# Performance work log

Measured on AMD Instinct MI355X. Metric: run time of the kernel, lower is better.

Reference implementation:

```python
import jax, jax.numpy as jnp
import numpy as np
from jax import lax

EMBED_DIM = 1024
NUM_HEADS = 8
KEY_DIM = EMBED_DIM // NUM_HEADS  # 128
B, H, W = 2, 48, 48
N = H * W


def _rope(t, sin, cos):
    # t: [..., d]; sin/cos broadcastable to t
    x1 = t[..., ::2]
    x2 = t[..., 1::2]
    rot = jnp.stack([-x2, x1], axis=-1).reshape(t.shape)  # interleave (-x2, x1)
    return t * cos - rot * sin


def setup_inputs() -> dict:
    key = jax.random.key(0)
    ks = jax.random.split(key, 16)
    C = EMBED_DIM
    w = 0.02
    return {
        "x": jax.random.normal(ks[0], (B, H, W, C), jnp.float32),
        "sin": jax.random.normal(ks[1], (H, W, KEY_DIM), jnp.float32),
        "cos": jax.random.normal(ks[2], (H, W, KEY_DIM), jnp.float32),
        "mask": jax.random.normal(ks[3], (NUM_HEADS, N, N), jnp.float32),
        "Wq": jax.random.normal(ks[4], (C, C), jnp.float32) * w,
        "bq": jax.random.normal(ks[5], (C,), jnp.float32) * w,
        "Wk": jax.random.normal(ks[6], (C, C), jnp.float32) * w,
        "bk": jax.random.normal(ks[7], (C,), jnp.float32) * w,
        "Wv": jax.random.normal(ks[8], (C, C), jnp.float32) * w,
        "bv": jax.random.normal(ks[9], (C,), jnp.float32) * w,
        "lepe_w": jax.random.normal(ks[10], (5, 5, 1, C), jnp.float32) * w,  # HWIO, groups=C
        "lepe_b": jax.random.normal(ks[11], (C,), jnp.float32) * w,
        "Wo": jax.random.normal(ks[12], (C, C), jnp.float32) * w,
        "bo": jnp.zeros((C,), jnp.float32),
    }


def reference(x, sin, cos, mask, Wq, bq, Wk, bk, Wv, bv, lepe_w, lepe_b, Wo, bo):
    Bb, Hh, Ww, C = x.shape
    nh, kd = NUM_HEADS, KEY_DIM
    scaling = kd ** -0.5

    q = x @ Wq.T + bq                     # [B,H,W,C]
    k = (x @ Wk.T + bk) * scaling         # [B,H,W,C]
    v = x @ Wv.T + bv                     # [B,H,W,C]

    # depthwise 5x5 lepe on NHWC
    lepe = lax.conv_general_dilated(
        v, lepe_w, window_strides=(1, 1), padding="SAME",
        dimension_numbers=("NHWC", "HWIO", "NHWC"),
        feature_group_count=C,
    ) + lepe_b

    # [B,H,W,C] -> [B,nh,H,W,kd]
    qh = q.reshape(Bb, Hh, Ww, nh, kd).transpose(0, 3, 1, 2, 4)
    kh = k.reshape(Bb, Hh, Ww, nh, kd).transpose(0, 3, 1, 2, 4)

    sin_ = sin[None, None]  # [1,1,H,W,kd]
    cos_ = cos[None, None]
    qh = _rope(qh, sin_, cos_)
    kh = _rope(kh, sin_, cos_)

    qf = qh.reshape(Bb, nh, Hh * Ww, kd)  # [B,nh,N,kd]
    kf = kh.reshape(Bb, nh, Hh * Ww, kd)
    vf = v.reshape(Bb, Hh, Ww, nh, kd).transpose(0, 3, 1, 2, 4).reshape(Bb, nh, Hh * Ww, kd)

    attn = jnp.einsum("bhnd,bhmd->bhnm", qf, kf) + mask  # [B,nh,N,N]
    attn = jax.nn.softmax(attn, axis=-1)
    out = jnp.einsum("bhnm,bhmd->bhnd", attn, vf)         # [B,nh,N,kd]

    out = out.transpose(0, 2, 1, 3).reshape(Bb, Hh, Ww, nh * kd)
    out = out + lepe
    return out @ Wo.T + bo
```

## Files before the change

kernel.cpp:

```cpp
#include <hip/hip_runtime.h>
#include <hip/hip_bf16.h>
#include <stdint.h>

typedef __bf16 bf16_t;
typedef __bf16 bf16x8 __attribute__((ext_vector_type(8)));
typedef __bf16 bf16x4 __attribute__((ext_vector_type(4)));
typedef float f32x4 __attribute__((ext_vector_type(4)));
typedef unsigned int u32x4 __attribute__((ext_vector_type(4)));

#define MFMA16(A, B, C) __builtin_amdgcn_mfma_f32_16x16x32_bf16(A, B, C, 0, 0, 0)

__device__ inline void dma16(const void* g, void* l) {
    __builtin_amdgcn_global_load_lds(
        (const __attribute__((address_space(1))) unsigned int*)g,
        (__attribute__((address_space(3))) unsigned int*)l, 16, 0, 0);
}

__device__ inline unsigned pack2(float a, float b) {
    unsigned short ua = __builtin_bit_cast(unsigned short, (bf16_t)a);
    unsigned short ub = __builtin_bit_cast(unsigned short, (bf16_t)b);
    return (unsigned)ua | ((unsigned)ub << 16);
}

__global__ __launch_bounds__(256)
void cvt_kernel(const float* __restrict__ in, bf16_t* __restrict__ outp, int n8)
{
    int i = blockIdx.x * 256 + threadIdx.x;
    if (i >= n8) return;
    const float* p = in + (size_t)i * 8;
    f32x4 a = *(const f32x4*)p;
    f32x4 b = *(const f32x4*)(p + 4);
    bf16x8 r;
    r[0] = (bf16_t)a[0]; r[1] = (bf16_t)a[1]; r[2] = (bf16_t)a[2]; r[3] = (bf16_t)a[3];
    r[4] = (bf16_t)b[0]; r[5] = (bf16_t)b[1]; r[6] = (bf16_t)b[2]; r[7] = (bf16_t)b[3];
    *(bf16x8*)(outp + (size_t)i * 8) = r;
}

__global__ __launch_bounds__(256)
void cvt4_kernel(const float* __restrict__ W0, const float* __restrict__ W1,
                 const float* __restrict__ W2, const float* __restrict__ W3,
                 bf16_t* __restrict__ outp)
{
    int i = blockIdx.x * 256 + threadIdx.x;
    int sel = i >> 17;
    int j = i & 131071;
    const float* src = sel == 0 ? W0 : sel == 1 ? W1 : sel == 2 ? W2 : W3;
    const float* p = src + (size_t)j * 8;
    f32x4 a = *(const f32x4*)p;
    f32x4 b = *(const f32x4*)(p + 4);
    bf16x8 r;
    r[0] = (bf16_t)a[0]; r[1] = (bf16_t)a[1]; r[2] = (bf16_t)a[2]; r[3] = (bf16_t)a[3];
    r[4] = (bf16_t)b[0]; r[5] = (bf16_t)b[1]; r[6] = (bf16_t)b[2]; r[7] = (bf16_t)b[3];
    *(bf16x8*)(outp + (size_t)i * 8) = r;
}

__device__ __forceinline__
void gemm_core(const bf16_t* __restrict__ A, const bf16_t* __restrict__ W,
               const float* __restrict__ bias, void* __restrict__ outp,
               int mode, float scale,
               const float* __restrict__ sinp, const float* __restrict__ cosp,
               int m0, int n0, char* lds)
{
    const int K = 1024;
    const int t = threadIdx.x;
    const int w = t >> 6, l = t & 63;
    const int wm = w >> 1, wn = w & 1;
    const int lr = l & 15;
    const int kch = (l >> 4) * 8;

    const f32x4 zz = {0.f, 0.f, 0.f, 0.f};
    f32x4 acc[4][4];
#pragma unroll
    for (int i = 0; i < 4; i++)
#pragma unroll
        for (int j = 0; j < 4; j++) acc[i][j] = zz;

#pragma unroll
    for (int i = 0; i < 2; i++) {
        int f = w * 2 + i;
        dma16(A + (size_t)(m0 + f * 16 + lr) * K + kch, lds + f * 1024);
        dma16(W + (size_t)(n0 + f * 16 + lr) * K + kch, lds + 8192 + f * 1024);
    }
    __syncthreads();

    int bo = 0;
    for (int k0 = 0; k0 < K; k0 += 32) {
        int kn = k0 + 32;
        if (kn < K) {
            int nb = bo ^ 16384;
#pragma unroll
            for (int i = 0; i < 2; i++) {
                int f = w * 2 + i;
                dma16(A + (size_t)(m0 + f * 16 + lr) * K + kn + kch, lds + nb + f * 1024);
                dma16(W + (size_t)(n0 + f * 16 + lr) * K + kn + kch, lds + nb + 8192 + f * 1024);
            }
        }
        bf16x8 af[4], bfg[4];
#pragma unroll
        for (int mt = 0; mt < 4; mt++)
            af[mt] = *(const bf16x8*)(lds + bo + ((wm * 4 + mt) * 64 + l) * 16);
#pragma unroll
        for (int nt = 0; nt < 4; nt++)
            bfg[nt] = *(const bf16x8*)(lds + bo + 8192 + ((wn * 4 + nt) * 64 + l) * 16);
#pragma unroll
        for (int mt = 0; mt < 4; mt++)
#pragma unroll
            for (int nt = 0; nt < 4; nt++)
                acc[mt][nt] = MFMA16(af[mt], bfg[nt], acc[mt][nt]);
        __syncthreads();
        bo ^= 16384;
    }

    const int quad = l >> 4, lc = l & 15;
#pragma unroll
    for (int mt = 0; mt < 4; mt++) {
#pragma unroll
        for (int nt = 0; nt < 4; nt++) {
            int gn = n0 + wn * 64 + nt * 16 + lc;
            float bv = bias[gn];
            int gm0 = m0 + wm * 64 + mt * 16 + quad * 4;
            if (mode == 0) {
                float* o32 = (float*)outp;
#pragma unroll
                for (int r = 0; r < 4; r++)
                    o32[(size_t)(gm0 + r) * 1024 + gn] = acc[mt][nt][r] + bv;
            } else if (mode == 1) {
                bf16_t* ob = (bf16_t*)outp;
                int h = gn >> 7, d = gn & 127;
#pragma unroll
                for (int r = 0; r < 4; r++) {
                    int gm = gm0 + r;
                    int b = gm / 2304;
                    int pos = gm - b * 2304;
                    float val = acc[mt][nt][r] + bv;
                    float pv = __shfl_xor(val, 1);
                    float sn = sinp[pos * 128 + d];
                    float cs = cosp[pos * 128 + d];
                    float res = (d & 1) ? (val * cs - pv * sn) : (val * cs + pv * sn);
                    ob[(((size_t)b * 8 + h) * 2304 + pos) * 128 + d] = (bf16_t)(res * scale);
                }
            } else {
                bf16_t* ob = (bf16_t*)outp;
                int h = gn >> 7, d = gn & 127;
                int b = gm0 / 2304;
                int pos0 = gm0 - b * 2304;
                bf16x4 s4;
#pragma unroll
                for (int r = 0; r < 4; r++)
                    s4[r] = (bf16_t)(acc[mt][nt][r] + bv);
                *(bf16x4*)(ob + (((size_t)b * 8 + h) * 128 + d) * 2304 + pos0) = s4;
            }
        }
    }
}

__global__ __launch_bounds__(256)
void gemm_bt_kernel(const bf16_t* __restrict__ A, const bf16_t* __restrict__ W,
                    const float* __restrict__ bias, void* __restrict__ outp,
                    int mode, float scale,
                    const float* __restrict__ sinp, const float* __restrict__ cosp)
{
    __shared__ __align__(16) char lds[32768];
    gemm_core(A, W, bias, outp, mode, scale, sinp, cosp,
              blockIdx.x * 128, blockIdx.y * 128, lds);
}

__global__ __launch_bounds__(256)
void gemm_qkv_kernel(const bf16_t* __restrict__ A, const bf16_t* __restrict__ Wall,
                     const float* __restrict__ bq, const float* __restrict__ bk,
                     const float* __restrict__ bv,
                     void* __restrict__ qb, void* __restrict__ kb, void* __restrict__ vtb,
                     const float* __restrict__ sinp, const float* __restrict__ cosp,
                     float kscale)
{
    __shared__ __align__(16) char lds[32768];
    int ny = blockIdx.y;
    int third = ny >> 3;
    int n0 = (ny & 7) * 128;
    const bf16_t* W = Wall + (size_t)third * 1048576;
    const float* bias = third == 0 ? bq : third == 1 ? bk : bv;
    void* outp = third == 0 ? qb : third == 1 ? kb : vtb;
    int mode = third == 2 ? 2 : 1;
    float scale = third == 1 ? kscale : 1.0f;
    gemm_core(A, W, bias, outp, mode, scale, sinp, cosp, blockIdx.x * 128, n0, lds);
}

__global__ __launch_bounds__(256)
void attn_kernel(const bf16_t* __restrict__ q, const bf16_t* __restrict__ k,
                 const bf16_t* __restrict__ vt, const float* __restrict__ mask,
                 bf16_t* __restrict__ o)
{
    const int N = 2304;
    __shared__ __align__(16) char lds[65536];

    const int t = threadIdx.x;
    const int w = t >> 6, l = t & 63;
    const int quad = l >> 4, lc = l & 15;

    const int bh = blockIdx.y;
    const int b = bh >> 3, h = bh & 7;
    const int q0 = blockIdx.x * 64;
    const int qrow = q0 + w * 16 + lc;

    const bf16_t* qb = q + (size_t)bh * N * 128;
    const bf16_t* kb = k + (size_t)bh * N * 128;
    const bf16_t* vtb = vt + (size_t)bh * 128 * N;
    const float* mq = mask + (size_t)h * N * N + (size_t)qrow * N + quad * 4;

    bf16x8 qf[4];
#pragma unroll
    for (int kc = 0; kc < 4; kc++)
        qf[kc] = *(const bf16x8*)(qb + (size_t)qrow * 128 + kc * 32 + quad * 8);

#pragma unroll
    for (int i = 0; i < 4; i++) {
        int f = w * 4 + i;
        dma16(kb + (size_t)((f >> 2) * 16 + lc) * 128 + (f & 3) * 32 + quad * 8,
              lds + f * 1024);
        dma16(vtb + (size_t)((f >> 1) * 16 + lc) * N + (f & 1) * 32 + quad * 8,
              lds + 16384 + f * 1024);
    }
    f32x4 mv[4];
#pragma unroll
    for (int nt = 0; nt < 4; nt++)
        mv[nt] = *(const f32x4*)(mq + nt * 16);
    __syncthreads();

    const f32x4 zz = {0.f, 0.f, 0.f, 0.f};
    float Mr = -1e30f, Lr = 0.f;
    f32x4 Oacc[8];
#pragma unroll
    for (int i = 0; i < 8; i++) Oacc[i] = zz;

    int bo = 0;
    for (int kv0 = 0; kv0 < N; kv0 += 64) {
        int nxt = kv0 + 64;
        f32x4 mvn[4];
        if (nxt < N) {
            int nb = bo ^ 32768;
#pragma unroll
            for (int i = 0; i < 4; i++) {
                int f = w * 4 + i;
                dma16(kb + (size_t)(nxt + (f >> 2) * 16 + lc) * 128 + (f & 3) * 32 + quad * 8,
                      lds + nb + f * 1024);
                dma16(vtb + (size_t)((f >> 1) * 16 + lc) * N + nxt + (f & 1) * 32 + quad * 8,
                      lds + nb + 16384 + f * 1024);
            }
#pragma unroll
            for (int nt = 0; nt < 4; nt++)
                mvn[nt] = *(const f32x4*)(mq + nxt + nt * 16);
        }

        const char* Ks = lds + bo;
        const char* Vts = lds + bo + 16384;

        f32x4 s[4];
#pragma unroll
        for (int nt = 0; nt < 4; nt++) {
            f32x4 a = zz;
#pragma unroll
            for (int kc = 0; kc < 4; kc++) {
                bf16x8 kf = *(const bf16x8*)(Ks + ((nt * 4 + kc) * 64 + l) * 16);
                a = MFMA16(kf, qf[kc], a);
            }
            s[nt] = a + mv[nt];
        }

        float mx = fmaxf(fmaxf(fmaxf(s[0][0], s[0][1]), fmaxf(s[0][2], s[0][3])),
                         fmaxf(fmaxf(s[1][0], s[1][1]), fmaxf(s[1][2], s[1][3])));
        mx = fmaxf(mx, fmaxf(fmaxf(fmaxf(s[2][0], s[2][1]), fmaxf(s[2][2], s[2][3])),
                             fmaxf(fmaxf(s[3][0], s[3][1]), fmaxf(s[3][2], s[3][3]))));
        mx = fmaxf(mx, __shfl_xor(mx, 16));
        mx = fmaxf(mx, __shfl_xor(mx, 32));
        float mnew = fmaxf(Mr, mx);
        float alpha = __expf(Mr - mnew);
        Mr = mnew;

        float rs = 0.f;
        unsigned pw[4][2];
#pragma unroll
        for (int nt = 0; nt < 4; nt++) {
            float p0 = __expf(s[nt][0] - mnew);
            float p1 = __expf(s[nt][1] - mnew);
            float p2 = __expf(s[nt][2] - mnew);
            float p3 = __expf(s[nt][3] - mnew);
            rs += (p0 + p1) + (p2 + p3);
            pw[nt][0] = pack2(p0, p1);
            pw[nt][1] = pack2(p2, p3);
        }
        rs += __shfl_xor(rs, 16);
        rs += __shfl_xor(rs, 32);
        Lr = Lr * alpha + rs;

#pragma unroll
        for (int dt = 0; dt < 8; dt++)
#pragma unroll
            for (int r = 0; r < 4; r++)
                Oacc[dt][r] *= alpha;

#pragma unroll
        for (int pc = 0; pc < 2; pc++) {
            u32x4 wv;
#pragma unroll
            for (int jp = 0; jp < 4; jp++) {
                int src = ((quad & 1) * 2 + (jp >> 1)) * 16 + lc;
                int t0 = __shfl((int)pw[pc * 2 + 0][jp & 1], src);
                int t1 = __shfl((int)pw[pc * 2 + 1][jp & 1], src);
                wv[jp] = (quad >> 1) ? (unsigned)t1 : (unsigned)t0;
            }
            bf16x8 pf = __builtin_bit_cast(bf16x8, wv);
#pragma unroll
            for (int dt = 0; dt < 8; dt++) {
                bf16x8 vf = *(const bf16x8*)(Vts + ((dt * 2 + pc) * 64 + l) * 16);
                Oacc[dt] = MFMA16(vf, pf, Oacc[dt]);
            }
        }

        __syncthreads();
        if (nxt < N) {
#pragma unroll
            for (int nt = 0; nt < 4; nt++) mv[nt] = mvn[nt];
            bo ^= 32768;
        }
    }

    float inv = 1.f / Lr;
#pragma unroll
    for (int dt = 0; dt < 8; dt++) {
        bf16x4 s4;
#pragma unroll
        for (int r = 0; r < 4; r++) s4[r] = (bf16_t)(Oacc[dt][r] * inv);
        *(bf16x4*)(o + ((size_t)b * N + qrow) * 1024 + h * 128 + dt * 16 + quad * 4) = s4;
    }
}

__global__ __launch_bounds__(256)
void lepe_kernel(const bf16_t* __restrict__ vt, const float* __restrict__ wgt,
                 const float* __restrict__ lb, const bf16_t* __restrict__ o,
                 bf16_t* __restrict__ ab)
{
    __shared__ __align__(16) bf16_t sv[5 * 48 * 128];
    const int bh = blockIdx.y;
    const int b = bh >> 3, h = bh & 7;
    const int y0 = blockIdx.x;
    const int t = threadIdx.x;

#pragma unroll
    for (int it = 0; it < 15; it++) {
        int idx = t + it * 256;
        int ck = idx % 6;
        int dy = idx / 6;
        int d = dy & 127, yloc = dy >> 7;
        int y = y0 - 2 + yloc;
        bf16x8 vvv;
#pragma unroll
        for (int j = 0; j < 8; j++) vvv[j] = (bf16_t)0.f;
        if (y >= 0 && y < 48)
            vvv = *(const bf16x8*)(vt + ((size_t)bh * 128 + d) * 2304 + y * 48 + ck * 8);
        int x0 = ck * 8;
#pragma unroll
        for (int j = 0; j < 8; j++)
            sv[(yloc * 48 + x0 + j) * 128 + d] = vvv[j];
    }
    __syncthreads();

    const int d0 = (t & 15) * 8;
    const int xb = t >> 4;
    float acc[3][8];
    f32x4 b0 = *(const f32x4*)(lb + h * 128 + d0);
    f32x4 b1 = *(const f32x4*)(lb + h * 128 + d0 + 4);
#pragma unroll
    for (int c = 0; c < 3; c++)
#pragma unroll
        for (int j = 0; j < 4; j++) { acc[c][j] = b0[j]; acc[c][4 + j] = b1[j]; }

#pragma unroll
    for (int ky = 0; ky < 5; ky++) {
#pragma unroll
        for (int kx = 0; kx < 5; kx++) {
            const float* wp = wgt + (size_t)(ky * 5 + kx) * 1024 + h * 128 + d0;
            f32x4 w0 = *(const f32x4*)wp;
            f32x4 w1 = *(const f32x4*)(wp + 4);
#pragma unroll
            for (int c = 0; c < 3; c++) {
                int xx = xb + c * 16 + kx - 2;
                if (xx < 0 || xx >= 48) continue;
                bf16x8 vv = *(const bf16x8*)(&sv[(ky * 48 + xx) * 128 + d0]);
#pragma unroll
                for (int j = 0; j < 4; j++) {
                    acc[c][j]     += (float)vv[j]     * w0[j];
                    acc[c][4 + j] += (float)vv[4 + j] * w1[j];
                }
            }
        }
    }
#pragma unroll
    for (int c = 0; c < 3; c++) {
        int x = xb + c * 16;
        size_t off = ((size_t)b * 2304 + y0 * 48 + x) * 1024 + h * 128 + d0;
        bf16x8 ov = *(const bf16x8*)(o + off);
        bf16x8 res;
#pragma unroll
        for (int j = 0; j < 8; j++) res[j] = (bf16_t)(acc[c][j] + (float)ov[j]);
        *(bf16x8*)(ab + off) = res;
    }
}

extern "C" void kernel_launch(void* const* d_in, const int* in_sizes, int n_in,
                              void* d_out, int out_size, void* d_ws, size_t ws_size,
                              hipStream_t stream)
{
    const float* x    = (const float*)d_in[0];
    const float* sin_ = (const float*)d_in[1];
    const float* cos_ = (const float*)d_in[2];
    const float* mask = (const float*)d_in[3];
    const float* Wq   = (const float*)d_in[4];
    const float* bq   = (const float*)d_in[5];
    const float* Wk   = (const float*)d_in[6];
    const float* bk   = (const float*)d_in[7];
    const float* Wv   = (const float*)d_in[8];
    const float* bv   = (const float*)d_in[9];
    const float* lw   = (const float*)d_in[10];
    const float* lb   = (const float*)d_in[11];
    const float* Wo   = (const float*)d_in[12];
    const float* bo   = (const float*)d_in[13];

    const size_t NB = (size_t)2 * 2304 * 1024;

    bf16_t* dout_b = (bf16_t*)d_out;
    bf16_t* x16 = dout_b;
    bf16_t* vtb = dout_b + NB;
    bf16_t* ob  = dout_b;

    bf16_t* qb   = (bf16_t*)d_ws;
    bf16_t* kb   = qb + NB;
    bf16_t* wbuf = kb + NB;
    bf16_t* ab   = qb;

    dim3 blk(256);
    const float kscale = 0.08838834764831845f;

    cvt_kernel<<<2304, blk, 0, stream>>>(x, x16, 589824);
    cvt4_kernel<<<2048, blk, 0, stream>>>(Wq, Wk, Wv, Wo, wbuf);
    gemm_qkv_kernel<<<dim3(36, 24), blk, 0, stream>>>(x16, wbuf, bq, bk, bv,
                                                      qb, kb, vtb, sin_, cos_, kscale);
    attn_kernel<<<dim3(36, 16), blk, 0, stream>>>(qb, kb, vtb, mask, ob);
    lepe_kernel<<<dim3(48, 16), blk, 0, stream>>>(vtb, lw, lb, ob, ab);
    gemm_bt_kernel<<<dim3(36, 8), blk, 0, stream>>>(ab, wbuf + 3 * 1048576, bo,
                                                    d_out, 0, 1.0f, nullptr, nullptr);
}
```

Measured before the change: 565.9 us.

## Split attention KV range across two wave groups and shrink GEMM M-tiles to 64

The attention kernel now runs 512 threads per block. Two groups of four waves each process half of the key/value sequence, and their partial softmax states (max, sum, output) are merged through LDS at the end. Blocks are also remapped so batch pairs sharing the same mask rows are adjacent, which aims to improve mask reuse in cache. The K/V double-buffer prefetch is replaced by a synchronous load for each tile, so the kernel now relies on more resident waves to hide latency. The GEMMs switch from 128-row to 64-row tiles, doubling the grid to improve CU occupancy, at the cost of less operand reuse per block.

```diff
diff --git a/kernel.cpp b/kernel.cpp
--- a/kernel.cpp
+++ b/kernel.cpp
@@ -55,13 +55,14 @@
 }
 
 __device__ __forceinline__
-void gemm_core(const bf16_t* __restrict__ A, const bf16_t* __restrict__ W,
-               const float* __restrict__ bias, void* __restrict__ outp,
-               int mode, float scale,
-               const float* __restrict__ sinp, const float* __restrict__ cosp,
-               int m0, int n0, char* lds)
+void gemm_core64(const bf16_t* __restrict__ A, const bf16_t* __restrict__ W,
+                 const float* __restrict__ bias, void* __restrict__ outp,
+                 int mode, float scale,
+                 const float* __restrict__ sinp, const float* __restrict__ cosp,
+                 int m0, int n0, char* lds)
 {
     const int K = 1024;
+    const int ASZ = 4096, BUF = 12288;
     const int t = threadIdx.x;
     const int w = t >> 6, l = t & 63;
     const int wm = w >> 1, wn = w & 1;
@@ -69,17 +70,17 @@
     const int kch = (l >> 4) * 8;
 
     const f32x4 zz = {0.f, 0.f, 0.f, 0.f};
-    f32x4 acc[4][4];
-#pragma unroll
-    for (int i = 0; i < 4; i++)
+    f32x4 acc[2][4];
+#pragma unroll
+    for (int i = 0; i < 2; i++)
 #pragma unroll
         for (int j = 0; j < 4; j++) acc[i][j] = zz;
 
+    dma16(A + (size_t)(m0 + w * 16 + lr) * K + kch, lds + w * 1024);
 #pragma unroll
     for (int i = 0; i < 2; i++) {
         int f = w * 2 + i;
-        dma16(A + (size_t)(m0 + f * 16 + lr) * K + kch, lds + f * 1024);
-        dma16(W + (size_t)(n0 + f * 16 + lr) * K + kch, lds + 8192 + f * 1024);
+        dma16(W + (size_t)(n0 + f * 16 + lr) * K + kch, lds + ASZ + f * 1024);
     }
     __syncthreads();
 
@@ -87,38 +88,38 @@
     for (int k0 = 0; k0 < K; k0 += 32) {
         int kn = k0 + 32;
         if (kn < K) {
-            int nb = bo ^ 16384;
+            int nb = bo ^ BUF;
+            dma16(A + (size_t)(m0 + w * 16 + lr) * K + kn + kch, lds + nb + w * 1024);
 #pragma unroll
             for (int i = 0; i < 2; i++) {
                 int f = w * 2 + i;
-                dma16(A + (size_t)(m0 + f * 16 + lr) * K + kn + kch, lds + nb + f * 1024);
-                dma16(W + (size_t)(n0 + f * 16 + lr) * K + kn + kch, lds + nb + 8192 + f * 1024);
-            }
-        }
-        bf16x8 af[4], bfg[4];
-#pragma unroll
-        for (int mt = 0; mt < 4; mt++)
-            af[mt] = *(const bf16x8*)(lds + bo + ((wm * 4 + mt) * 64 + l) * 16);
+                dma16(W + (size_t)(n0 + f * 16 + lr) * K + kn + kch, lds + nb + ASZ + f * 1024);
+            }
+        }
+        bf16x8 af[2], bfg[4];
+#pragma unroll
+        for (int mt = 0; mt < 2; mt++)
+            af[mt] = *(const bf16x8*)(lds + bo + ((wm * 2 + mt) * 64 + l) * 16);
 #pragma unroll
         for (int nt = 0; nt < 4; nt++)
-            bfg[nt] = *(const bf16x8*)(lds + bo + 8192 + ((wn * 4 + nt) * 64 + l) * 16);
-#pragma unroll
-        for (int mt = 0; mt < 4; mt++)
+            bfg[nt] = *(const bf16x8*)(lds + bo + ASZ + ((wn * 4 + nt) * 64 + l) * 16);
+#pragma unroll
+        for (int mt = 0; mt < 2; mt++)
 #pragma unroll
             for (int nt = 0; nt < 4; nt++)
                 acc[mt][nt] = MFMA16(af[mt], bfg[nt], acc[mt][nt]);
         __syncthreads();
-        bo ^= 16384;
+        bo ^= BUF;
     }
 
     const int quad = l >> 4, lc = l & 15;
 #pragma unroll
-    for (int mt = 0; mt < 4; mt++) {
+    for (int mt = 0; mt < 2; mt++) {
 #pragma unroll
         for (int nt = 0; nt < 4; nt++) {
             int gn = n0 + wn * 64 + nt * 16 + lc;
             float bv = bias[gn];
-            int gm0 = m0 + wm * 64 + mt * 16 + quad * 4;
+            int gm0 = m0 + wm * 32 + mt * 16 + quad * 4;
             if (mode == 0) {
                 float* o32 = (float*)outp;
 #pragma unroll
@@ -160,9 +161,9 @@
                     int mode, float scale,
                     const float* __restrict__ sinp, const float* __restrict__ cosp)
 {
-    __shared__ __align__(16) char lds[32768];
-    gemm_core(A, W, bias, outp, mode, scale, sinp, cosp,
-              blockIdx.x * 128, blockIdx.y * 128, lds);
+    __shared__ __align__(16) char lds[24576];
+    gemm_core64(A, W, bias, outp, mode, scale, sinp, cosp,
+                blockIdx.x * 64, blockIdx.y * 128, lds);
 }
 
 __global__ __launch_bounds__(256)
@@ -173,7 +174,7 @@
                      const float* __restrict__ sinp, const float* __restrict__ cosp,
                      float kscale)
 {
-    __shared__ __align__(16) char lds[32768];
+    __shared__ __align__(16) char lds[24576];
     int ny = blockIdx.y;
     int third = ny >> 3;
     int n0 = (ny & 7) * 128;
@@ -182,49 +183,50 @@
     void* outp = third == 0 ? qb : third == 1 ? kb : vtb;
     int mode = third == 2 ? 2 : 1;
     float scale = third == 1 ? kscale : 1.0f;
-    gemm_core(A, W, bias, outp, mode, scale, sinp, cosp, blockIdx.x * 128, n0, lds);
-}
-
-__global__ __launch_bounds__(256)
+    gemm_core64(A, W, bias, outp, mode, scale, sinp, cosp, blockIdx.x * 64, n0, lds);
+}
+
+__global__ __launch_bounds__(512, 4)
 void attn_kernel(const bf16_t* __restrict__ q, const bf16_t* __restrict__ k,
                  const bf16_t* __restrict__ vt, const float* __restrict__ mask,
                  bf16_t* __restrict__ o)
 {
     const int N = 2304;
+    const int HK = 1152;
     __shared__ __align__(16) char lds[65536];
 
     const int t = threadIdx.x;
     const int w = t >> 6, l = t & 63;
+    const int hv = w >> 2, wl = w & 3;
     const int quad = l >> 4, lc = l & 15;
 
-    const int bh = blockIdx.y;
-    const int b = bh >> 3, h = bh & 7;
-    const int q0 = blockIdx.x * 64;
-    const int qrow = q0 + w * 16 + lc;
+    int gid = blockIdx.x;
+    int grp = gid >> 4, sub = gid & 15;
+    int u = grp * 8 + (sub & 7);
+    int b = sub >> 3;
+    int qblk = u >> 3, h = u & 7;
+    int bh = b * 8 + h;
+    int q0 = qblk * 64;
+
+    const int qrow = q0 + wl * 16 + lc;
 
     const bf16_t* qb = q + (size_t)bh * N * 128;
-    const bf16_t* kb = k + (size_t)bh * N * 128;
-    const bf16_t* vtb = vt + (size_t)bh * 128 * N;
-    const float* mq = mask + (size_t)h * N * N + (size_t)qrow * N + quad * 4;
+    const bf16_t* kb = k + (size_t)bh * N * 128 + (size_t)hv * HK * 128;
+    const bf16_t* vtb = vt + (size_t)bh * 128 * N + hv * HK;
+    const float* mq = mask + (size_t)h * N * N + (size_t)qrow * N + hv * HK + quad * 4;
+
+    char* Ks = lds + hv * 32768;
+    char* Vts = Ks + 16384;
 
     bf16x8 qf[4];
 #pragma unroll
     for (int kc = 0; kc < 4; kc++)
         qf[kc] = *(const bf16x8*)(qb + (size_t)qrow * 128 + kc * 32 + quad * 8);
 
-#pragma unroll
-    for (int i = 0; i < 4; i++) {
-        int f = w * 4 + i;
-        dma16(kb + (size_t)((f >> 2) * 16 + lc) * 128 + (f & 3) * 32 + quad * 8,
-              lds + f * 1024);
-        dma16(vtb + (size_t)((f >> 1) * 16 + lc) * N + (f & 1) * 32 + quad * 8,
-              lds + 16384 + f * 1024);
-    }
-    f32x4 mv[4];
+    f32x4 mv[4], mvn[4];
 #pragma unroll
     for (int nt = 0; nt < 4; nt++)
         mv[nt] = *(const f32x4*)(mq + nt * 16);
-    __syncthreads();
 
     const f32x4 zz = {0.f, 0.f, 0.f, 0.f};
     float Mr = -1e30f, Lr = 0.f;
@@ -232,27 +234,23 @@
 #pragma unroll
     for (int i = 0; i < 8; i++) Oacc[i] = zz;
 
-    int bo = 0;
-    for (int kv0 = 0; kv0 < N; kv0 += 64) {
+    for (int kv0 = 0; kv0 < HK; kv0 += 64) {
+        __syncthreads();
+#pragma unroll
+        for (int i = 0; i < 4; i++) {
+            int f = wl * 4 + i;
+            dma16(kb + (size_t)(kv0 + (f >> 2) * 16 + lc) * 128 + (f & 3) * 32 + quad * 8,
+                  Ks + f * 1024);
+            dma16(vtb + (size_t)((f >> 1) * 16 + lc) * N + kv0 + (f & 1) * 32 + quad * 8,
+                  Vts + f * 1024);
+        }
+        __syncthreads();
         int nxt = kv0 + 64;
-        f32x4 mvn[4];
-        if (nxt < N) {
-            int nb = bo ^ 32768;
-#pragma unroll
-            for (int i = 0; i < 4; i++) {
-                int f = w * 4 + i;
-                dma16(kb + (size_t)(nxt + (f >> 2) * 16 + lc) * 128 + (f & 3) * 32 + quad * 8,
-                      lds + nb + f * 1024);
-                dma16(vtb + (size_t)((f >> 1) * 16 + lc) * N + nxt + (f & 1) * 32 + quad * 8,
-                      lds + nb + 16384 + f * 1024);
-            }
+        if (nxt < HK) {
 #pragma unroll
             for (int nt = 0; nt < 4; nt++)
                 mvn[nt] = *(const f32x4*)(mq + nxt + nt * 16);
         }
-
-        const char* Ks = lds + bo;
-        const char* Vts = lds + bo + 16384;
 
         f32x4 s[4];
 #pragma unroll
@@ -316,21 +314,41 @@
             }
         }
 
-        __syncthreads();
-        if (nxt < N) {
+        if (nxt < HK) {
 #pragma unroll
             for (int nt = 0; nt < 4; nt++) mv[nt] = mvn[nt];
-            bo ^= 32768;
-        }
-    }
-
-    float inv = 1.f / Lr;
-#pragma unroll
-    for (int dt = 0; dt < 8; dt++) {
-        bf16x4 s4;
-#pragma unroll
-        for (int r = 0; r < 4; r++) s4[r] = (bf16_t)(Oacc[dt][r] * inv);
-        *(bf16x4*)(o + ((size_t)b * N + qrow) * 1024 + h * 128 + dt * 16 + quad * 4) = s4;
+        }
+    }
+
+    __syncthreads();
+    float* Ml = (float*)(lds + 32768);
+    if (hv == 1) {
+        float* ob = (float*)(lds + wl * 8192);
+#pragma unroll
+        for (int dt = 0; dt < 8; dt++)
+            *(f32x4*)(ob + (size_t)(dt * 64 + l) * 4) = Oacc[dt];
+        if (quad == 0) {
+            Ml[wl * 16 + lc] = Mr;
+            Ml[64 + wl * 16 + lc] = Lr;
+        }
+    }
+    __syncthreads();
+    if (hv == 0) {
+        const float* ob = (const float*)(lds + wl * 8192);
+        float M1 = Ml[wl * 16 + lc];
+        float L1 = Ml[64 + wl * 16 + lc];
+        float M = fmaxf(Mr, M1);
+        float w0 = __expf(Mr - M), w1 = __expf(M1 - M);
+        float inv = 1.f / (Lr * w0 + L1 * w1);
+#pragma unroll
+        for (int dt = 0; dt < 8; dt++) {
+            f32x4 o1 = *(const f32x4*)(ob + (size_t)(dt * 64 + l) * 4);
+            bf16x4 s4;
+#pragma unroll
+            for (int r = 0; r < 4; r++)
+                s4[r] = (bf16_t)((Oacc[dt][r] * w0 + o1[r] * w1) * inv);
+            *(bf16x4*)(o + ((size_t)b * N + qrow) * 1024 + h * 128 + dt * 16 + quad * 4) = s4;
+        }
     }
 }
 
@@ -442,10 +460,10 @@
 
     cvt_kernel<<<2304, blk, 0, stream>>>(x, x16, 589824);
     cvt4_kernel<<<2048, blk, 0, stream>>>(Wq, Wk, Wv, Wo, wbuf);
-    gemm_qkv_kernel<<<dim3(36, 24), blk, 0, stream>>>(x16, wbuf, bq, bk, bv,
+    gemm_qkv_kernel<<<dim3(72, 24), blk, 0, stream>>>(x16, wbuf, bq, bk, bv,
                                                       qb, kb, vtb, sin_, cos_, kscale);
-    attn_kernel<<<dim3(36, 16), blk, 0, stream>>>(qb, kb, vtb, mask, ob);
+    attn_kernel<<<576, dim3(512), 0, stream>>>(qb, kb, vtb, mask, ob);
     lepe_kernel<<<dim3(48, 16), blk, 0, stream>>>(vtb, lw, lb, ob, ab);
-    gemm_bt_kernel<<<dim3(36, 8), blk, 0, stream>>>(ab, wbuf + 3 * 1048576, bo,
+    gemm_bt_kernel<<<dim3(72, 8), blk, 0, stream>>>(ab, wbuf + 3 * 1048576, bo,
                                                     d_out, 0, 1.0f, nullptr, nullptr);
 }
```

Result: no change. 571.9 us (+1.1%).
